# Performance work log

Measured on AMD Instinct MI355X. Metric: run time of the kernel, lower is better.

## Reference

```python
import jax, jax.numpy as jnp
import numpy as np

NA, NW, H = 20000, 100000, 128
DA, DW = 64, 128
E_CR, E_IN, E_CO = 400000, 600000, 300000


def _seg_softmax(logits, seg, n):
    m = jax.ops.segment_max(logits, seg, num_segments=n)
    e = jnp.exp(logits - m[seg])
    s = jax.ops.segment_sum(e, seg, num_segments=n)
    return e / (s[seg] + 1e-16)


def _gat(x_src, x_dst, edge, W, b, a_s, a_d):
    # PyG GATConv, heads=1, concat=False, shared lin for src/dst, add_self_loops=True
    n_src, n_dst = x_src.shape[0], x_dst.shape[0]
    loops = jnp.arange(min(n_src, n_dst), dtype=edge.dtype)
    src = jnp.concatenate([edge[0], loops])
    dst = jnp.concatenate([edge[1], loops])
    hs = x_src @ W            # [n_src, H]
    hd = x_dst @ W            # [n_dst, H]
    logit = jax.nn.leaky_relu((hs @ a_s)[src] + (hd @ a_d)[dst], 0.2)
    alpha = _seg_softmax(logit, dst, n_dst)          # softmax over in-neighborhoods
    out = jax.ops.segment_sum(alpha[:, None] * hs[src], dst, num_segments=n_dst)
    return out + b


def _mlp2(x, w1, b1, w2, b2):
    return jax.nn.relu(x @ w1 + b1) @ w2 + b2


def setup_inputs() -> dict:
    key = jax.random.key(0)
    ks = iter(jax.random.split(key, 40))

    def p(shape, scale=0.1):
        return jax.random.normal(next(ks), shape, jnp.float32) * scale

    def edges(n_src, n_dst, E):
        s = jax.random.randint(next(ks), (E,), 0, n_src, dtype=jnp.int32)
        d = jax.random.randint(next(ks), (E,), 0, n_dst, dtype=jnp.int32)
        d = jnp.where(s == d, (d + 1) % n_dst, d)  # keep input loop-free (PyG strips them)
        return jnp.stack([s, d])

    e_creates = edges(NA, NW, E_CR)
    inp = {
        'artist_feat': jax.random.normal(next(ks), (NA, DA), jnp.float32),
        'work_feat': jax.random.normal(next(ks), (NW, DW), jnp.float32),
        'a_w1': p((DA, H)), 'a_b1': jnp.zeros(H, jnp.float32),
        'a_w2': p((H, H)), 'a_b2': jnp.zeros(H, jnp.float32),
        'w_w1': p((DW, H)), 'w_b1': jnp.zeros(H, jnp.float32),
        'w_w2': p((H, H)), 'w_b2': jnp.zeros(H, jnp.float32),
        'cr_W': p((H, H)), 'cr_b': jnp.zeros(H, jnp.float32), 'cr_as': p((H,)), 'cr_ad': p((H,)),
        'in_W': p((H, H)), 'in_b': jnp.zeros(H, jnp.float32), 'in_as': p((H,)), 'in_ad': p((H,)),
        'co_W': p((H, H)), 'co_b': jnp.zeros(H, jnp.float32), 'co_as': p((H,)), 'co_ad': p((H,)),
        'p_w1': p((2 * H, 256)), 'p_b1': jnp.zeros(256, jnp.float32),
        'p_w2': p((256, 128)), 'p_b2': jnp.zeros(128, jnp.float32),
        'p_w3': p((128, 1)), 'p_b3': jnp.zeros(1, jnp.float32),
        'e_creates': e_creates,
        'e_created_by': jnp.flip(e_creates, axis=0),  # reverse relation [work, artist]
        'e_infl': edges(NW, NW, E_IN),
        'e_collab': edges(NA, NA, E_CO),
    }
    return inp


def reference(artist_feat, work_feat,
              a_w1, a_b1, a_w2, a_b2,
              w_w1, w_b1, w_w2, w_b2,
              cr_W, cr_b, cr_as, cr_ad,
              in_W, in_b, in_as, in_ad,
              co_W, co_b, co_as, co_ad,
              p_w1, p_b1, p_w2, p_b2, p_w3, p_b3,
              e_creates, e_created_by, e_infl, e_collab):
    ax = _mlp2(artist_feat, a_w1, a_b1, a_w2, a_b2)      # [NA, H]
    wx = _mlp2(work_feat, w_w1, w_b1, w_w2, w_b2)        # [NW, H]
    wx = jax.nn.elu(_gat(ax, wx, e_creates, cr_W, cr_b, cr_as, cr_ad))
    wx = jax.nn.elu(_gat(wx, wx, e_infl, in_W, in_b, in_as, in_ad))
    au = _gat(wx, ax, e_created_by, cr_W, cr_b, cr_as, cr_ad)  # no elu (matches source)
    ac = jax.nn.elu(_gat(au, au, e_collab, co_W, co_b, co_as, co_ad))
    comb = jnp.concatenate([au, ac], axis=1)             # [NA, 2H]
    h = jax.nn.relu(comb @ p_w1 + p_b1)                  # dropout is identity in eval
    h = jax.nn.relu(h @ p_w2 + p_b2)
    return (h @ p_w3 + p_b3).squeeze()
```

## Files before the change

### kernel.cpp

```cpp
#include <hip/hip_runtime.h>
#include <hip/hip_bf16.h>
#include <cstddef>

#define NA 20000
#define NW 100000
#define HH 128
#define DA 64
#define E_CR 400000
#define E_IN 600000
#define E_CO 300000

#define ROW1 0
#define ROW2 (NW)
#define ROW3 (2 * NW)
#define ROW4 (2 * NW + NA)
#define NTOT (2 * NW + 2 * NA)
#define CAPW 40
#define CAPA 88
#define NPREP (10 * 128 + 1)

typedef short v8s __attribute__((ext_vector_type(8)));
typedef float v4f __attribute__((ext_vector_type(4)));

constexpr int PSLOT = 2 * 128 * 264;

__device__ inline short f2bf(float x) {
    union { float f; unsigned u; } c; c.f = x;
    unsigned r = c.u + 0x7fff + ((c.u >> 16) & 1);
    return (short)(r >> 16);
}
__device__ inline float bf2f(short s) {
    union { unsigned u; float f; } c; c.u = ((unsigned)(unsigned short)s) << 16;
    return c.f;
}
__device__ inline float bfu2f(unsigned short s) {
    union { unsigned u; float f; } c; c.u = ((unsigned)s) << 16;
    return c.f;
}

__device__ inline void split8(const float* xv, v8s& h, v8s& l) {
#pragma unroll
    for (int p = 0; p < 4; ++p) {
        float2 xf; xf.x = xv[2 * p]; xf.y = xv[2 * p + 1];
        __hip_bfloat162 hb = __float22bfloat162_rn(xf);
        float2 hf = __bfloat1622float2(hb);
        float2 lf; lf.x = xf.x - hf.x; lf.y = xf.y - hf.y;
        __hip_bfloat162 lb = __float22bfloat162_rn(lf);
        union { __hip_bfloat162 b; short2 s; } uh, ul;
        uh.b = hb; ul.b = lb;
        h[2 * p] = uh.s.x; h[2 * p + 1] = uh.s.y;
        l[2 * p] = ul.s.x; l[2 * p + 1] = ul.s.y;
    }
}

struct AppChunk { const int* e; int E; int* pad; int cap; int* deg; };

__device__ inline void do_append(const AppChunk& ap, int bid) {
    int b0 = bid * 1024 + threadIdx.x;
    int s[4], d[4]; bool ok[4];
#pragma unroll
    for (int u = 0; u < 4; ++u) {
        int i = b0 + u * 256;
        ok[u] = i < ap.E;
        s[u] = 0; d[u] = 0;
        if (ok[u]) { s[u] = ap.e[i]; d[u] = ap.e[ap.E + i]; }
    }
    int p[4];
#pragma unroll
    for (int u = 0; u < 4; ++u) if (ok[u]) p[u] = atomicAdd(&ap.deg[d[u]], 1);
#pragma unroll
    for (int u = 0; u < 4; ++u)
        if (ok[u] && p[u] < ap.cap)
            ap.pad[(size_t)d[u] * ap.cap + p[u]] = s[u];
}

struct PrepDesc { const float* src; int ldw; int K; };
struct PrepArgs { PrepDesc d[10]; const float* wvW; const float* wvA; float* vd; };

__global__ __launch_bounds__(256) void k_prep_append(PrepArgs a, short* __restrict__ out,
                                                    AppChunk ap)
{
    if (blockIdx.x >= NPREP) { do_append(ap, blockIdx.x - NPREP); return; }
    if (blockIdx.x == NPREP - 1) {
        __shared__ float sa[HH];
        int t = threadIdx.x;
        if (t < HH) sa[t] = a.wvA[t];
        __syncthreads();
        if (t < HH) {
            float s = 0.f;
            for (int jj = 0; jj < HH; ++jj) s += a.wvW[(size_t)t * HH + jj] * sa[jj];
            a.vd[t] = s;
        }
        return;
    }
    int m = blockIdx.x >> 7;
    int e = (blockIdx.x & 127) * 256 + threadIdx.x;
    PrepDesc dd = a.d[m];
    int K = dd.K;
    int KP = (K <= 128) ? K + 8 : K;
    if (e >= K * 128) return;
    int n = e & 127, k = e >> 7;
    float x = dd.src[(size_t)k * dd.ldw + n];
    short h = f2bf(x);
    short l = f2bf(x - bf2f(h));
    short* base = out + (size_t)m * PSLOT;
    base[n * KP + k] = h;
    base[128 * KP + n * KP + k] = l;
}

template<int K, int ACT, int NSS, int ST, int LDSB, int OBF, int DUAL>
__global__ __launch_bounds__(256, 2) void k_mfma(
    const float* __restrict__ X, int ldx,
    const short* __restrict__ Wp,
    const float* __restrict__ bias,
    float* __restrict__ Y, int ldy, int M,
    const float* __restrict__ v1, float* __restrict__ ss1,
    const float* __restrict__ v2, float* __restrict__ ss2,
    const float* __restrict__ sb)
{
    constexpr int KF = K / 32;
    constexpr int KP = LDSB ? K + 8 : K;
    __shared__ short Bs[LDSB ? 2 * 128 * (K + 8) : 8];
    const int tid = threadIdx.x;
    const int wave = tid >> 6, lane = tid & 63;
    const int l15 = lane & 15, quad = lane >> 4;
    int bid = blockIdx.x;
    if (DUAL) {
        int g0 = gridDim.x >> 1;
        if (bid >= g0) { bid -= g0; Wp += PSLOT; bias += 128; Y += 128; }
    }
    const int wrow = bid * 128 + wave * 32;

    if (LDSB) {
        const float4* src = (const float4*)Wp;
        float4* dst = (float4*)Bs;
        constexpr int total = 2 * 128 * KP / 8;
        for (int i = tid; i < total; i += 256) dst[i] = src[i];
    }

    v4f acc[2][8];
#pragma unroll
    for (int rf = 0; rf < 2; ++rf)
#pragma unroll
        for (int cf = 0; cf < 8; ++cf) acc[rf][cf] = (v4f){0.f, 0.f, 0.f, 0.f};

    if (LDSB) {
        v8s ah[2][KF], al[2][KF];
#pragma unroll
        for (int rf = 0; rf < 2; ++rf) {
            int r = wrow + rf * 16 + l15; if (r >= M) r = M - 1;
            const float* xp = X + (size_t)r * ldx + quad * 8;
#pragma unroll
            for (int kf = 0; kf < KF; ++kf) {
                float xv[8];
                *(float4*)&xv[0] = *(const float4*)(xp + kf * 32);
                *(float4*)&xv[4] = *(const float4*)(xp + kf * 32 + 4);
                split8(xv, ah[rf][kf], al[rf][kf]);
            }
        }
        __syncthreads();
#pragma unroll
        for (int kf = 0; kf < KF; ++kf) {
#pragma unroll
            for (int cf = 0; cf < 8; ++cf) {
                const short* bp = &Bs[(cf * 16 + l15) * KP + kf * 32 + quad * 8];
                v8s bh = *(const v8s*)bp;
                v8s bl = *(const v8s*)(bp + 128 * KP);
#pragma unroll
                for (int rf = 0; rf < 2; ++rf) {
                    acc[rf][cf] = __builtin_amdgcn_mfma_f32_16x16x32_bf16(al[rf][kf], bh, acc[rf][cf], 0, 0, 0);
                    acc[rf][cf] = __builtin_amdgcn_mfma_f32_16x16x32_bf16(ah[rf][kf], bl, acc[rf][cf], 0, 0, 0);
                    acc[rf][cf] = __builtin_amdgcn_mfma_f32_16x16x32_bf16(ah[rf][kf], bh, acc[rf][cf], 0, 0, 0);
                }
            }
        }
    } else {
        for (int kf = 0; kf < KF; ++kf) {
            v8s ah[2], al[2];
#pragma unroll
            for (int rf = 0; rf < 2; ++rf) {
                int r = wrow + rf * 16 + l15; if (r >= M) r = M - 1;
                const float* xp = X + (size_t)r * ldx + kf * 32 + quad * 8;
                float xv[8];
                *(float4*)&xv[0] = *(const float4*)xp;
                *(float4*)&xv[4] = *(const float4*)(xp + 4);
                split8(xv, ah[rf], al[rf]);
            }
#pragma unroll
            for (int cf = 0; cf < 8; ++cf) {
                const short* bp = Wp + (size_t)(cf * 16 + l15) * K + kf * 32 + quad * 8;
                v8s bh = *(const v8s*)bp;
                v8s bl = *(const v8s*)(bp + 128 * KP);
#pragma unroll
                for (int rf = 0; rf < 2; ++rf) {
                    acc[rf][cf] = __builtin_amdgcn_mfma_f32_16x16x32_bf16(al[rf], bh, acc[rf][cf], 0, 0, 0);
                    acc[rf][cf] = __builtin_amdgcn_mfma_f32_16x16x32_bf16(ah[rf], bl, acc[rf][cf], 0, 0, 0);
                    acc[rf][cf] = __builtin_amdgcn_mfma_f32_16x16x32_bf16(ah[rf], bh, acc[rf][cf], 0, 0, 0);
                }
            }
        }
    }

    float bv[8], v1c[8], v2c[8];
#pragma unroll
    for (int cf = 0; cf < 8; ++cf) {
        int col = cf * 16 + l15;
        bv[cf] = bias ? bias[col] : 0.f;
        if (NSS >= 1) v1c[cf] = v1[col];
        if (NSS >= 2) v2c[cf] = v2[col];
    }
    float sbv = (NSS >= 1 && sb) ? sb[0] : 0.f;

#pragma unroll
    for (int rf = 0; rf < 2; ++rf) {
#pragma unroll
        for (int reg = 0; reg < 4; ++reg) {
            int r = wrow + rf * 16 + quad * 4 + reg;
            if (r >= M) continue;
            float p1 = 0.f, p2 = 0.f;
#pragma unroll
            for (int cf = 0; cf < 8; ++cf) {
                float o = acc[rf][cf][reg] + bv[cf];
                if (ACT == 1) o = o > 0.f ? o : 0.f;
                if (NSS >= 1) p1 = fmaf(o, v1c[cf], p1);
                if (NSS >= 2) p2 = fmaf(o, v2c[cf], p2);
                if (ST) {
                    if (OBF) ((unsigned short*)Y)[(size_t)r * ldy + cf * 16 + l15] = (unsigned short)f2bf(o);
                    else     Y[(size_t)r * ldy + cf * 16 + l15] = o;
                }
            }
            if (NSS >= 1) {
#pragma unroll
                for (int w = 1; w < 16; w <<= 1) {
                    p1 += __shfl_xor(p1, w, 64);
                    if (NSS >= 2) p2 += __shfl_xor(p2, w, 64);
                }
                if (l15 == 0) {
                    ss1[r] = p1 + sbv;
                    if (NSS >= 2) ss2[r] = p2;
                }
            }
        }
    }
}

struct MfmaCfg {
    const float* X; int ldx;
    const short* Wp;
    const float* bias;
    float* Y; int ldy; int M;
    int act, nss, obf;
    const float* v1; float* ss1;
    const float* v2; float* ss2;
    int nblocks;
};

__global__ __launch_bounds__(256, 2) void k_mfma2(MfmaCfg c0, MfmaCfg c1, AppChunk ap)
{
    constexpr int K = 128, KF = 4, KP = 136;
    __shared__ short Bs[2 * 128 * KP];
    int bid = blockIdx.x;
    if (bid >= c0.nblocks + c1.nblocks) { do_append(ap, bid - c0.nblocks - c1.nblocks); return; }
    const bool first = bid < c0.nblocks;
    const MfmaCfg& c = first ? c0 : c1;
    if (!first) bid -= c0.nblocks;
    const int tid = threadIdx.x;
    const int wave = tid >> 6, lane = tid & 63;
    const int l15 = lane & 15, quad = lane >> 4;
    const int wrow = bid * 128 + wave * 32;

    {
        const float4* src = (const float4*)c.Wp;
        float4* dst = (float4*)Bs;
        constexpr int total = 2 * 128 * KP / 8;
        for (int i = tid; i < total; i += 256) dst[i] = src[i];
    }

    v4f acc[2][8];
#pragma unroll
    for (int rf = 0; rf < 2; ++rf)
#pragma unroll
        for (int cf = 0; cf < 8; ++cf) acc[rf][cf] = (v4f){0.f, 0.f, 0.f, 0.f};

    v8s ah[2][KF], al[2][KF];
#pragma unroll
    for (int rf = 0; rf < 2; ++rf) {
        int r = wrow + rf * 16 + l15; if (r >= c.M) r = c.M - 1;
        const float* xp = c.X + (size_t)r * c.ldx + quad * 8;
#pragma unroll
        for (int kf = 0; kf < KF; ++kf) {
            float xv[8];
            *(float4*)&xv[0] = *(const float4*)(xp + kf * 32);
            *(float4*)&xv[4] = *(const float4*)(xp + kf * 32 + 4);
            split8(xv, ah[rf][kf], al[rf][kf]);
        }
    }
    __syncthreads();
#pragma unroll
    for (int kf = 0; kf < KF; ++kf) {
#pragma unroll
        for (int cf = 0; cf < 8; ++cf) {
            const short* bp = &Bs[(cf * 16 + l15) * KP + kf * 32 + quad * 8];
            v8s bh = *(const v8s*)bp;
            v8s bl = *(const v8s*)(bp + 128 * KP);
#pragma unroll
            for (int rf = 0; rf < 2; ++rf) {
                acc[rf][cf] = __builtin_amdgcn_mfma_f32_16x16x32_bf16(al[rf][kf], bh, acc[rf][cf], 0, 0, 0);
                acc[rf][cf] = __builtin_amdgcn_mfma_f32_16x16x32_bf16(ah[rf][kf], bl, acc[rf][cf], 0, 0, 0);
                acc[rf][cf] = __builtin_amdgcn_mfma_f32_16x16x32_bf16(ah[rf][kf], bh, acc[rf][cf], 0, 0, 0);
            }
        }
    }

    float bv[8], v1c[8], v2c[8];
#pragma unroll
    for (int cf = 0; cf < 8; ++cf) {
        int col = cf * 16 + l15;
        bv[cf] = c.bias ? c.bias[col] : 0.f;
        v1c[cf] = (c.nss >= 1) ? c.v1[col] : 0.f;
        v2c[cf] = (c.nss >= 2) ? c.v2[col] : 0.f;
    }

#pragma unroll
    for (int rf = 0; rf < 2; ++rf) {
#pragma unroll
        for (int reg = 0; reg < 4; ++reg) {
            int r = wrow + rf * 16 + quad * 4 + reg;
            if (r >= c.M) continue;
            float p1 = 0.f, p2 = 0.f;
#pragma unroll
            for (int cf = 0; cf < 8; ++cf) {
                float o = acc[rf][cf][reg] + bv[cf];
                if (c.act) o = o > 0.f ? o : 0.f;
                p1 = fmaf(o, v1c[cf], p1);
                p2 = fmaf(o, v2c[cf], p2);
                if (c.obf) ((unsigned short*)c.Y)[(size_t)r * c.ldy + cf * 16 + l15] = (unsigned short)f2bf(o);
                else       c.Y[(size_t)r * c.ldy + cf * 16 + l15] = o;
            }
            if (c.nss >= 1) {
#pragma unroll
                for (int w = 1; w < 16; w <<= 1) {
                    p1 += __shfl_xor(p1, w, 64);
                    p2 += __shfl_xor(p2, w, 64);
                }
                if (l15 == 0) {
                    c.ss1[r] = p1;
                    if (c.nss >= 2) c.ss2[r] = p2;
                }
            }
        }
    }
}

template<int ELU, int U, int CAP>
__global__ __launch_bounds__(256) void k_aggregate(
    const int* __restrict__ deg, const int* __restrict__ esp,
    const unsigned short* __restrict__ hs, const float* __restrict__ ss,
    const float* __restrict__ sd, const float* __restrict__ bias,
    float* __restrict__ out, int ldy, int n, int loopn)
{
    int lane = threadIdx.x & 63;
    int wv = threadIdx.x >> 6;
    int d = blockIdx.x * 4 + wv;
    if (d >= n) return;
    int half = lane >> 5;
    int col = (lane & 31) * 4;
    const int* row = esp + (size_t)d * CAP;
    int i1 = deg[d]; if (i1 > CAP) i1 = CAP;
    float sdv = sd[d];
    float den = 0.f;
    float ax = 0.f, ay = 0.f, az = 0.f, aw = 0.f;
    if (half == 0 && d < loopn) {
        ushort4 h = *(const ushort4*)(hs + (size_t)d * HH + col);
        float l = ss[d] + sdv;
        l = l < 0.f ? 0.2f * l : l;
        float e = __expf(l);
        den += e;
        ax = fmaf(e, bfu2f(h.x), ax);
        ay = fmaf(e, bfu2f(h.y), ay);
        az = fmaf(e, bfu2f(h.z), az);
        aw = fmaf(e, bfu2f(h.w), aw);
    }
    int i = 0;
    for (; i + 2 * U <= i1; i += 2 * U) {
        int s[U]; ushort4 h[U]; float sv[U];
#pragma unroll
        for (int u = 0; u < U; ++u) s[u] = row[i + 2 * u + half];
#pragma unroll
        for (int u = 0; u < U; ++u) h[u] = *(const ushort4*)(hs + (size_t)s[u] * HH + col);
#pragma unroll
        for (int u = 0; u < U; ++u) sv[u] = ss[s[u]];
#pragma unroll
        for (int u = 0; u < U; ++u) {
            float l = sv[u] + sdv;
            l = l < 0.f ? 0.2f * l : l;
            float e = __expf(l);
            den += e;
            ax = fmaf(e, bfu2f(h[u].x), ax);
            ay = fmaf(e, bfu2f(h[u].y), ay);
            az = fmaf(e, bfu2f(h[u].z), az);
            aw = fmaf(e, bfu2f(h[u].w), aw);
        }
    }
    if (i < i1) {
        int s[U]; ushort4 h[U]; float sv[U]; bool act[U];
#pragma unroll
        for (int u = 0; u < U; ++u) {
            int idx = i + 2 * u + half;
            act[u] = idx < i1;
            s[u] = row[act[u] ? idx : (i1 - 1)];
        }
#pragma unroll
        for (int u = 0; u < U; ++u) h[u] = *(const ushort4*)(hs + (size_t)s[u] * HH + col);
#pragma unroll
        for (int u = 0; u < U; ++u) sv[u] = ss[s[u]];
#pragma unroll
        for (int u = 0; u < U; ++u) {
            float l = sv[u] + sdv;
            l = l < 0.f ? 0.2f * l : l;
            float e = act[u] ? __expf(l) : 0.f;
            den += e;
            ax = fmaf(e, bfu2f(h[u].x), ax);
            ay = fmaf(e, bfu2f(h[u].y), ay);
            az = fmaf(e, bfu2f(h[u].z), az);
            aw = fmaf(e, bfu2f(h[u].w), aw);
        }
    }
    den += __shfl_xor(den, 32, 64);
    ax += __shfl_xor(ax, 32, 64);
    ay += __shfl_xor(ay, 32, 64);
    az += __shfl_xor(az, 32, 64);
    aw += __shfl_xor(aw, 32, 64);
    if (half == 0) {
        float4 b = *(const float4*)(bias + col);
        float inv = 1.f / (den + 1e-16f);
        float o0 = ax * inv + b.x;
        float o1 = ay * inv + b.y;
        float o2 = az * inv + b.z;
        float o3 = aw * inv + b.w;
        if (ELU) {
            o0 = o0 > 0.f ? o0 : expm1f(o0);
            o1 = o1 > 0.f ? o1 : expm1f(o1);
            o2 = o2 > 0.f ? o2 : expm1f(o2);
            o3 = o3 > 0.f ? o3 : expm1f(o3);
        }
        *(float4*)(out + (size_t)d * ldy + col) = make_float4(o0, o1, o2, o3);
    }
}

extern "C" void kernel_launch(void* const* d_in, const int* in_sizes, int n_in,
                              void* d_out, int out_size, void* d_ws, size_t ws_size,
                              hipStream_t stream)
{
    const float* artist = (const float*)d_in[0];
    const float* workf  = (const float*)d_in[1];
    const float* a_w1 = (const float*)d_in[2];  const float* a_b1 = (const float*)d_in[3];
    const float* a_w2 = (const float*)d_in[4];  const float* a_b2 = (const float*)d_in[5];
    const float* w_w1 = (const float*)d_in[6];  const float* w_b1 = (const float*)d_in[7];
    const float* w_w2 = (const float*)d_in[8];  const float* w_b2 = (const float*)d_in[9];
    const float* cr_W = (const float*)d_in[10]; const float* cr_b = (const float*)d_in[11];
    const float* cr_as = (const float*)d_in[12]; const float* cr_ad = (const float*)d_in[13];
    const float* in_W = (const float*)d_in[14]; const float* in_b = (const float*)d_in[15];
    const float* in_as = (const float*)d_in[16]; const float* in_ad = (const float*)d_in[17];
    const float* co_W = (const float*)d_in[18]; const float* co_b = (const float*)d_in[19];
    const float* co_as = (const float*)d_in[20]; const float* co_ad = (const float*)d_in[21];
    const float* p_w1 = (const float*)d_in[22]; const float* p_b1 = (const float*)d_in[23];
    const float* p_w2 = (const float*)d_in[24]; const float* p_b2 = (const float*)d_in[25];
    const float* p_w3 = (const float*)d_in[26]; const float* p_b3 = (const float*)d_in[27];
    const int* e_cr = (const int*)d_in[28];
    const int* e_cb = (const int*)d_in[29];
    const int* e_in = (const int*)d_in[30];
    const int* e_co = (const int*)d_in[31];

    char* wsp = (char*)d_ws;
    size_t off = 0;
    auto alloc = [&](size_t bytes) -> void* {
        void* p = wsp + off;
        off += (bytes + 255) / 256 * 256;
        return p;
    };
    float* ax   = (float*)alloc((size_t)NA * HH * 4);
    float* hsA  = (float*)alloc((size_t)NA * HH * 4);
    float* wx   = (float*)alloc((size_t)NW * HH * 4);
    float* hs   = (float*)alloc((size_t)NW * HH * 4);
    unsigned short* hsb = (unsigned short*)alloc((size_t)NW * HH * 2);
    float* comb = (float*)alloc((size_t)NA * 256 * 4);
    float* ss1 = (float*)alloc((size_t)NA * 4);
    float* sd1 = (float*)alloc((size_t)NW * 4);
    float* ss2 = (float*)alloc((size_t)NW * 4);
    float* sd2 = (float*)alloc((size_t)NW * 4);
    float* ss3 = (float*)alloc((size_t)NW * 4);
    float* sd3 = (float*)alloc((size_t)NA * 4);
    float* ss4 = (float*)alloc((size_t)NA * 4);
    float* sd4 = (float*)alloc((size_t)NA * 4);
    float* vd  = (float*)alloc(HH * 4);
    int* deg   = (int*)alloc((size_t)NTOT * 4);
    int* pad1  = (int*)alloc((size_t)NW * CAPW * 4);
    int* pad2  = (int*)alloc((size_t)NW * CAPW * 4);
    int* pad3  = (int*)alloc((size_t)NA * CAPA * 4);
    int* pad4  = (int*)alloc((size_t)NA * CAPA * 4);
    short* preW = (short*)alloc((size_t)10 * PSLOT * 2);
    (void)ws_size; (void)in_sizes; (void)n_in; (void)out_size;

    auto pre = [&](int m) { return preW + (size_t)m * PSLOT; };
    auto gg = [](int M) { return (M + 127) / 128; };
    auto apb = [](int E) { return (E + 1023) / 1024; };
    const float* nf = nullptr;
    float* nfm = nullptr;

    PrepArgs pa;
    pa.d[0] = {a_w1, HH, DA};
    pa.d[1] = {a_w2, HH, HH};
    pa.d[2] = {w_w1, HH, HH};
    pa.d[3] = {w_w2, HH, HH};
    pa.d[4] = {cr_W, HH, HH};
    pa.d[5] = {in_W, HH, HH};
    pa.d[6] = {co_W, HH, HH};
    pa.d[7] = {p_w1, 256, 256};
    pa.d[8] = {p_w1 + 128, 256, 256};
    pa.d[9] = {p_w2, HH, 256};
    pa.wvW = cr_W; pa.wvA = cr_ad; pa.vd = vd;

    AppChunk ap1 = {e_cr, E_CR, pad1, CAPW, deg + ROW1};
    AppChunk ap2 = {e_in, E_IN, pad2, CAPW, deg + ROW2};
    AppChunk ap3 = {e_cb, E_CR, pad3, CAPA, deg + ROW3};
    AppChunk ap4 = {e_co, E_CO, pad4, CAPA, deg + ROW4};
    AppChunk ap0 = {nullptr, 0, nullptr, 1, nullptr};

    (void)hipMemsetAsync(deg, 0, (size_t)NTOT * 4, stream);

    k_prep_append<<<NPREP + apb(E_CR), 256, 0, stream>>>(pa, preW, ap1);

    k_mfma<DA, 1, 0, 1, 1, 0, 0><<<gg(NA), 256, 0, stream>>>(artist, DA, pre(0), a_b1, hsA, HH, NA, nf, nfm, nf, nfm, nf);

    {
        MfmaCfg c0 = {workf, HH, pre(2), w_b1, hs, HH, NW, 1, 0, 0, nf, nfm, nf, nfm, gg(NW)};
        MfmaCfg c1 = {hsA, HH, pre(1), a_b2, ax, HH, NA, 0, 1, 0, vd, sd3, nf, nfm, gg(NA)};
        k_mfma2<<<gg(NW) + gg(NA) + apb(E_IN), 256, 0, stream>>>(c0, c1, ap2);
    }
    {
        MfmaCfg c0 = {hs, HH, pre(3), w_b2, wx, HH, NW, 0, 1, 0, vd, sd1, nf, nfm, gg(NW)};
        MfmaCfg c1 = {ax, HH, pre(4), nullptr, (float*)hsb, HH, NA, 0, 1, 1, cr_as, ss1, nf, nfm, gg(NA)};
        k_mfma2<<<gg(NW) + gg(NA) + apb(E_CR), 256, 0, stream>>>(c0, c1, ap3);
    }

    k_aggregate<1, 2, CAPW><<<(NW + 3) / 4, 256, 0, stream>>>(deg + ROW1, pad1, hsb, ss1, sd1, cr_b, wx, HH, NW, NA);

    {
        MfmaCfg c0 = {wx, HH, pre(5), nullptr, (float*)hsb, HH, NW, 0, 2, 1, in_as, ss2, in_ad, sd2, gg(NW)};
        MfmaCfg c1 = {nullptr, 0, nullptr, nullptr, nullptr, 0, 0, 0, 0, 0, nf, nfm, nf, nfm, 0};
        k_mfma2<<<gg(NW) + apb(E_CO), 256, 0, stream>>>(c0, c1, ap4);
    }
    k_aggregate<1, 2, CAPW><<<(NW + 3) / 4, 256, 0, stream>>>(deg + ROW2, pad2, hsb, ss2, sd2, in_b, wx, HH, NW, NW);

    k_mfma<HH, 0, 1, 1, 1, 1, 0><<<gg(NW), 256, 0, stream>>>(wx, HH, pre(4), nullptr, (float*)hsb, HH, NW, cr_as, ss3, nf, nfm, nf);
    k_aggregate<0, 4, CAPA><<<(NA + 3) / 4, 256, 0, stream>>>(deg + ROW3, pad3, hsb, ss3, sd3, cr_b, comb, 256, NA, NA);

    k_mfma<HH, 0, 2, 1, 1, 1, 0><<<gg(NA), 256, 0, stream>>>(comb, 256, pre(6), nullptr, (float*)hsb, HH, NA, co_as, ss4, co_ad, sd4, nf);
    k_aggregate<1, 4, CAPA><<<(NA + 3) / 4, 256, 0, stream>>>(deg + ROW4, pad4, hsb, ss4, sd4, co_b, comb + 128, 256, NA, NA);

    float* h1 = hs;
    k_mfma<256, 1, 0, 1, 0, 0, 1><<<2 * gg(NA), 256, 0, stream>>>(comb, 256, pre(7), p_b1, h1, 256, NA, nf, nfm, nf, nfm, nf);
    k_mfma<256, 1, 1, 0, 0, 0, 0><<<gg(NA), 256, 0, stream>>>(h1, 256, pre(9), p_b2, nfm, 0, NA, p_w3, (float*)d_out, nf, nfm, p_b3);
}
```

Measured before the change: 588.0 us.

## Halve GEMM LDS use, widen aggregate gathers to 8 bf16, rebalance edge appends

The MFMA kernels now stage only the high bf16 half of the split weights in LDS and read the low half straight from global memory, halving shared memory per block. The aggregate kernel switches from two 32-lane halves with 4-wide loads to four 16-lane quarters with 8-wide (16-byte) loads, with unroll factors reduced to match. Edge-append work is rebalanced: the influence edges are split across two fused launches via lo/hi ranges, and the artist-side projection becomes a k_mfma2 that also absorbs an append chunk. The aim is higher occupancy and better gather efficiency, at the cost of extra global/L2 traffic for the low-half weights and more cross-lane shuffles.

```diff
diff --git a/kernel.cpp b/kernel.cpp
--- a/kernel.cpp
+++ b/kernel.cpp
@@ -20,6 +20,7 @@
 #define NPREP (10 * 128 + 1)
 
 typedef short v8s __attribute__((ext_vector_type(8)));
+typedef unsigned short v8us __attribute__((ext_vector_type(8)));
 typedef float v4f __attribute__((ext_vector_type(4)));
 
 constexpr int PSLOT = 2 * 128 * 264;
@@ -53,15 +54,15 @@
     }
 }
 
-struct AppChunk { const int* e; int E; int* pad; int cap; int* deg; };
+struct AppChunk { const int* e; int E; int lo, hi; int* pad; int cap; int* deg; };
 
 __device__ inline void do_append(const AppChunk& ap, int bid) {
-    int b0 = bid * 1024 + threadIdx.x;
+    int b0 = ap.lo + bid * 1024 + threadIdx.x;
     int s[4], d[4]; bool ok[4];
 #pragma unroll
     for (int u = 0; u < 4; ++u) {
         int i = b0 + u * 256;
-        ok[u] = i < ap.E;
+        ok[u] = i < ap.hi;
         s[u] = 0; d[u] = 0;
         if (ok[u]) { s[u] = ap.e[i]; d[u] = ap.e[ap.E + i]; }
     }
@@ -120,7 +121,7 @@
 {
     constexpr int KF = K / 32;
     constexpr int KP = LDSB ? K + 8 : K;
-    __shared__ short Bs[LDSB ? 2 * 128 * (K + 8) : 8];
+    __shared__ short Bs[LDSB ? 128 * (K + 8) : 8];
     const int tid = threadIdx.x;
     const int wave = tid >> 6, lane = tid & 63;
     const int l15 = lane & 15, quad = lane >> 4;
@@ -134,7 +135,7 @@
     if (LDSB) {
         const float4* src = (const float4*)Wp;
         float4* dst = (float4*)Bs;
-        constexpr int total = 2 * 128 * KP / 8;
+        constexpr int total = 128 * KP / 8;
         for (int i = tid; i < total; i += 256) dst[i] = src[i];
     }
 
@@ -163,9 +164,9 @@
         for (int kf = 0; kf < KF; ++kf) {
 #pragma unroll
             for (int cf = 0; cf < 8; ++cf) {
-                const short* bp = &Bs[(cf * 16 + l15) * KP + kf * 32 + quad * 8];
-                v8s bh = *(const v8s*)bp;
-                v8s bl = *(const v8s*)(bp + 128 * KP);
+                int coff = (cf * 16 + l15) * KP + kf * 32 + quad * 8;
+                v8s bh = *(const v8s*)&Bs[coff];
+                v8s bl = *(const v8s*)(Wp + 128 * KP + coff);
 #pragma unroll
                 for (int rf = 0; rf < 2; ++rf) {
                     acc[rf][cf] = __builtin_amdgcn_mfma_f32_16x16x32_bf16(al[rf][kf], bh, acc[rf][cf], 0, 0, 0);
@@ -257,8 +258,8 @@
 
 __global__ __launch_bounds__(256, 2) void k_mfma2(MfmaCfg c0, MfmaCfg c1, AppChunk ap)
 {
-    constexpr int K = 128, KF = 4, KP = 136;
-    __shared__ short Bs[2 * 128 * KP];
+    constexpr int KF = 4, KP = 136;
+    __shared__ short Bs[128 * KP];
     int bid = blockIdx.x;
     if (bid >= c0.nblocks + c1.nblocks) { do_append(ap, bid - c0.nblocks - c1.nblocks); return; }
     const bool first = bid < c0.nblocks;
@@ -272,7 +273,7 @@
     {
         const float4* src = (const float4*)c.Wp;
         float4* dst = (float4*)Bs;
-        constexpr int total = 2 * 128 * KP / 8;
+        constexpr int total = 128 * KP / 8;
         for (int i = tid; i < total; i += 256) dst[i] = src[i];
     }
 
@@ -300,9 +301,9 @@
     for (int kf = 0; kf < KF; ++kf) {
 #pragma unroll
         for (int cf = 0; cf < 8; ++cf) {
-            const short* bp = &Bs[(cf * 16 + l15) * KP + kf * 32 + quad * 8];
-            v8s bh = *(const v8s*)bp;
-            v8s bl = *(const v8s*)(bp + 128 * KP);
+            int coff = (cf * 16 + l15) * KP + kf * 32 + quad * 8;
+            v8s bh = *(const v8s*)&Bs[coff];
+            v8s bl = *(const v8s*)(c.Wp + 128 * KP + coff);
 #pragma unroll
             for (int rf = 0; rf < 2; ++rf) {
                 acc[rf][cf] = __builtin_amdgcn_mfma_f32_16x16x32_bf16(al[rf][kf], bh, acc[rf][cf], 0, 0, 0);
@@ -363,31 +364,31 @@
     int wv = threadIdx.x >> 6;
     int d = blockIdx.x * 4 + wv;
     if (d >= n) return;
-    int half = lane >> 5;
-    int col = (lane & 31) * 4;
+    int q = lane >> 4;
+    int col = (lane & 15) * 8;
     const int* row = esp + (size_t)d * CAP;
     int i1 = deg[d]; if (i1 > CAP) i1 = CAP;
     float sdv = sd[d];
     float den = 0.f;
-    float ax = 0.f, ay = 0.f, az = 0.f, aw = 0.f;
-    if (half == 0 && d < loopn) {
-        ushort4 h = *(const ushort4*)(hs + (size_t)d * HH + col);
+    float acc[8];
+#pragma unroll
+    for (int j = 0; j < 8; ++j) acc[j] = 0.f;
+    if (q == 0 && d < loopn) {
+        v8us h = *(const v8us*)(hs + (size_t)d * HH + col);
         float l = ss[d] + sdv;
         l = l < 0.f ? 0.2f * l : l;
         float e = __expf(l);
         den += e;
-        ax = fmaf(e, bfu2f(h.x), ax);
-        ay = fmaf(e, bfu2f(h.y), ay);
-        az = fmaf(e, bfu2f(h.z), az);
-        aw = fmaf(e, bfu2f(h.w), aw);
+#pragma unroll
+        for (int j = 0; j < 8; ++j) acc[j] = fmaf(e, bfu2f(h[j]), acc[j]);
     }
     int i = 0;
-    for (; i + 2 * U <= i1; i += 2 * U) {
-        int s[U]; ushort4 h[U]; float sv[U];
-#pragma unroll
-        for (int u = 0; u < U; ++u) s[u] = row[i + 2 * u + half];
-#pragma unroll
-        for (int u = 0; u < U; ++u) h[u] = *(const ushort4*)(hs + (size_t)s[u] * HH + col);
+    for (; i + 4 * U <= i1; i += 4 * U) {
+        int s[U]; v8us h[U]; float sv[U];
+#pragma unroll
+        for (int u = 0; u < U; ++u) s[u] = row[i + 4 * u + q];
+#pragma unroll
+        for (int u = 0; u < U; ++u) h[u] = *(const v8us*)(hs + (size_t)s[u] * HH + col);
 #pragma unroll
         for (int u = 0; u < U; ++u) sv[u] = ss[s[u]];
 #pragma unroll
@@ -396,22 +397,20 @@
             l = l < 0.f ? 0.2f * l : l;
             float e = __expf(l);
             den += e;
-            ax = fmaf(e, bfu2f(h[u].x), ax);
-            ay = fmaf(e, bfu2f(h[u].y), ay);
-            az = fmaf(e, bfu2f(h[u].z), az);
-            aw = fmaf(e, bfu2f(h[u].w), aw);
+#pragma unroll
+            for (int j = 0; j < 8; ++j) acc[j] = fmaf(e, bfu2f(h[u][j]), acc[j]);
         }
     }
     if (i < i1) {
-        int s[U]; ushort4 h[U]; float sv[U]; bool act[U];
+        int s[U]; v8us h[U]; float sv[U]; bool act[U];
 #pragma unroll
         for (int u = 0; u < U; ++u) {
-            int idx = i + 2 * u + half;
+            int idx = i + 4 * u + q;
             act[u] = idx < i1;
             s[u] = row[act[u] ? idx : (i1 - 1)];
         }
 #pragma unroll
-        for (int u = 0; u < U; ++u) h[u] = *(const ushort4*)(hs + (size_t)s[u] * HH + col);
+        for (int u = 0; u < U; ++u) h[u] = *(const v8us*)(hs + (size_t)s[u] * HH + col);
 #pragma unroll
         for (int u = 0; u < U; ++u) sv[u] = ss[s[u]];
 #pragma unroll
@@ -420,31 +419,27 @@
             l = l < 0.f ? 0.2f * l : l;
             float e = act[u] ? __expf(l) : 0.f;
             den += e;
-            ax = fmaf(e, bfu2f(h[u].x), ax);
-            ay = fmaf(e, bfu2f(h[u].y), ay);
-            az = fmaf(e, bfu2f(h[u].z), az);
-            aw = fmaf(e, bfu2f(h[u].w), aw);
-        }
-    }
+#pragma unroll
+            for (int j = 0; j < 8; ++j) acc[j] = fmaf(e, bfu2f(h[u][j]), acc[j]);
+        }
+    }
+    den += __shfl_xor(den, 16, 64);
     den += __shfl_xor(den, 32, 64);
-    ax += __shfl_xor(ax, 32, 64);
-    ay += __shfl_xor(ay, 32, 64);
-    az += __shfl_xor(az, 32, 64);
-    aw += __shfl_xor(aw, 32, 64);
-    if (half == 0) {
-        float4 b = *(const float4*)(bias + col);
+#pragma unroll
+    for (int j = 0; j < 8; ++j) {
+        acc[j] += __shfl_xor(acc[j], 16, 64);
+        acc[j] += __shfl_xor(acc[j], 32, 64);
+    }
+    if (q == 0) {
         float inv = 1.f / (den + 1e-16f);
-        float o0 = ax * inv + b.x;
-        float o1 = ay * inv + b.y;
-        float o2 = az * inv + b.z;
-        float o3 = aw * inv + b.w;
-        if (ELU) {
-            o0 = o0 > 0.f ? o0 : expm1f(o0);
-            o1 = o1 > 0.f ? o1 : expm1f(o1);
-            o2 = o2 > 0.f ? o2 : expm1f(o2);
-            o3 = o3 > 0.f ? o3 : expm1f(o3);
-        }
-        *(float4*)(out + (size_t)d * ldy + col) = make_float4(o0, o1, o2, o3);
+        float o[8];
+#pragma unroll
+        for (int j = 0; j < 8; ++j) {
+            o[j] = acc[j] * inv + bias[col + j];
+            if (ELU) o[j] = o[j] > 0.f ? o[j] : expm1f(o[j]);
+        }
+        *(float4*)(out + (size_t)d * ldy + col) = *(float4*)&o[0];
+        *(float4*)(out + (size_t)d * ldy + col + 4) = *(float4*)&o[4];
     }
 }
 
@@ -504,7 +499,7 @@
 
     auto pre = [&](int m) { return preW + (size_t)m * PSLOT; };
     auto gg = [](int M) { return (M + 127) / 128; };
-    auto apb = [](int E) { return (E + 1023) / 1024; };
+    auto apb = [](int lo, int hi) { return (hi - lo + 1023) / 1024; };
     const float* nf = nullptr;
     float* nfm = nullptr;
 
@@ -521,43 +516,48 @@
     pa.d[9] = {p_w2, HH, 256};
     pa.wvW = cr_W; pa.wvA = cr_ad; pa.vd = vd;
 
-    AppChunk ap1 = {e_cr, E_CR, pad1, CAPW, deg + ROW1};
-    AppChunk ap2 = {e_in, E_IN, pad2, CAPW, deg + ROW2};
-    AppChunk ap3 = {e_cb, E_CR, pad3, CAPA, deg + ROW3};
-    AppChunk ap4 = {e_co, E_CO, pad4, CAPA, deg + ROW4};
-    AppChunk ap0 = {nullptr, 0, nullptr, 1, nullptr};
+    const int EHALF = 300000;
+    AppChunk ap1  = {e_cr, E_CR, 0, E_CR, pad1, CAPW, deg + ROW1};
+    AppChunk ap2a = {e_in, E_IN, 0, EHALF, pad2, CAPW, deg + ROW2};
+    AppChunk ap2b = {e_in, E_IN, EHALF, E_IN, pad2, CAPW, deg + ROW2};
+    AppChunk ap3  = {e_cb, E_CR, 0, E_CR, pad3, CAPA, deg + ROW3};
+    AppChunk ap4  = {e_co, E_CO, 0, E_CO, pad4, CAPA, deg + ROW4};
 
     (void)hipMemsetAsync(deg, 0, (size_t)NTOT * 4, stream);
 
-    k_prep_append<<<NPREP + apb(E_CR), 256, 0, stream>>>(pa, preW, ap1);
+    k_prep_append<<<NPREP + apb(0, E_CR), 256, 0, stream>>>(pa, preW, ap1);
 
     k_mfma<DA, 1, 0, 1, 1, 0, 0><<<gg(NA), 256, 0, stream>>>(artist, DA, pre(0), a_b1, hsA, HH, NA, nf, nfm, nf, nfm, nf);
 
     {
         MfmaCfg c0 = {workf, HH, pre(2), w_b1, hs, HH, NW, 1, 0, 0, nf, nfm, nf, nfm, gg(NW)};
         MfmaCfg c1 = {hsA, HH, pre(1), a_b2, ax, HH, NA, 0, 1, 0, vd, sd3, nf, nfm, gg(NA)};
-        k_mfma2<<<gg(NW) + gg(NA) + apb(E_IN), 256, 0, stream>>>(c0, c1, ap2);
+        k_mfma2<<<gg(NW) + gg(NA) + apb(0, EHALF), 256, 0, stream>>>(c0, c1, ap2a);
     }
     {
         MfmaCfg c0 = {hs, HH, pre(3), w_b2, wx, HH, NW, 0, 1, 0, vd, sd1, nf, nfm, gg(NW)};
         MfmaCfg c1 = {ax, HH, pre(4), nullptr, (float*)hsb, HH, NA, 0, 1, 1, cr_as, ss1, nf, nfm, gg(NA)};
-        k_mfma2<<<gg(NW) + gg(NA) + apb(E_CR), 256, 0, stream>>>(c0, c1, ap3);
-    }
-
-    k_aggregate<1, 2, CAPW><<<(NW + 3) / 4, 256, 0, stream>>>(deg + ROW1, pad1, hsb, ss1, sd1, cr_b, wx, HH, NW, NA);
+        k_mfma2<<<gg(NW) + gg(NA) + apb(EHALF, E_IN), 256, 0, stream>>>(c0, c1, ap2b);
+    }
+
+    k_aggregate<1, 1, CAPW><<<(NW + 3) / 4, 256, 0, stream>>>(deg + ROW1, pad1, hsb, ss1, sd1, cr_b, wx, HH, NW, NA);
 
     {
         MfmaCfg c0 = {wx, HH, pre(5), nullptr, (float*)hsb, HH, NW, 0, 2, 1, in_as, ss2, in_ad, sd2, gg(NW)};
         MfmaCfg c1 = {nullptr, 0, nullptr, nullptr, nullptr, 0, 0, 0, 0, 0, nf, nfm, nf, nfm, 0};
-        k_mfma2<<<gg(NW) + apb(E_CO), 256, 0, stream>>>(c0, c1, ap4);
-    }
-    k_aggregate<1, 2, CAPW><<<(NW + 3) / 4, 256, 0, stream>>>(deg + ROW2, pad2, hsb, ss2, sd2, in_b, wx, HH, NW, NW);
-
-    k_mfma<HH, 0, 1, 1, 1, 1, 0><<<gg(NW), 256, 0, stream>>>(wx, HH, pre(4), nullptr, (float*)hsb, HH, NW, cr_as, ss3, nf, nfm, nf);
-    k_aggregate<0, 4, CAPA><<<(NA + 3) / 4, 256, 0, stream>>>(deg + ROW3, pad3, hsb, ss3, sd3, cr_b, comb, 256, NA, NA);
+        k_mfma2<<<gg(NW) + apb(0, E_CR), 256, 0, stream>>>(c0, c1, ap3);
+    }
+    k_aggregate<1, 1, CAPW><<<(NW + 3) / 4, 256, 0, stream>>>(deg + ROW2, pad2, hsb, ss2, sd2, in_b, wx, HH, NW, NW);
+
+    {
+        MfmaCfg c0 = {wx, HH, pre(4), nullptr, (float*)hsb, HH, NW, 0, 1, 1, cr_as, ss3, nf, nfm, gg(NW)};
+        MfmaCfg c1 = {nullptr, 0, nullptr, nullptr, nullptr, 0, 0, 0, 0, 0, nf, nfm, nf, nfm, 0};
+        k_mfma2<<<gg(NW) + apb(0, E_CO), 256, 0, stream>>>(c0, c1, ap4);
+    }
+    k_aggregate<0, 2, CAPA><<<(NA + 3) / 4, 256, 0, stream>>>(deg + ROW3, pad3, hsb, ss3, sd3, cr_b, comb, 256, NA, NA);
 
     k_mfma<HH, 0, 2, 1, 1, 1, 0><<<gg(NA), 256, 0, stream>>>(comb, 256, pre(6), nullptr, (float*)hsb, HH, NA, co_as, ss4, co_ad, sd4, nf);
-    k_aggregate<1, 4, CAPA><<<(NA + 3) / 4, 256, 0, stream>>>(deg + ROW4, pad4, hsb, ss4, sd4, co_b, comb + 128, 256, NA, NA);
+    k_aggregate<1, 2, CAPA><<<(NA + 3) / 4, 256, 0, stream>>>(deg + ROW4, pad4, hsb, ss4, sd4, co_b, comb + 128, 256, NA, NA);
 
     float* h1 = hs;
     k_mfma<256, 1, 0, 1, 0, 0, 1><<<2 * gg(NA), 256, 0, stream>>>(comb, 256, pre(7), p_b1, h1, 256, NA, nf, nfm, nf, nfm, nf);
```

Measured after the change: 688.3 us. +17.1%, slower.

## Rebalance edge-append work across fused GEMM launches and halve LDS weight staging

Applied to the files above, without the earlier changes.

The edge-bucketing (append) work is redistributed. The influence edges are split into two halves that piggyback on the first two fused GEMM launches, and the created_by and collab appends move to later GEMM launches (the latter now a fused k_mfma2 launch). Separately, only the high bf16 half of the split weights is staged in LDS, while the low half is read straight from global memory. This halves shared memory per block, which may allow more blocks per CU, at the cost of extra global or L2 loads in the MFMA inner loop.

```diff
diff --git a/kernel.cpp b/kernel.cpp
--- a/kernel.cpp
+++ b/kernel.cpp
@@ -53,15 +53,15 @@
     }
 }
 
-struct AppChunk { const int* e; int E; int* pad; int cap; int* deg; };
+struct AppChunk { const int* e; int E; int lo, hi; int* pad; int cap; int* deg; };
 
 __device__ inline void do_append(const AppChunk& ap, int bid) {
-    int b0 = bid * 1024 + threadIdx.x;
+    int b0 = ap.lo + bid * 1024 + threadIdx.x;
     int s[4], d[4]; bool ok[4];
 #pragma unroll
     for (int u = 0; u < 4; ++u) {
         int i = b0 + u * 256;
-        ok[u] = i < ap.E;
+        ok[u] = i < ap.hi;
         s[u] = 0; d[u] = 0;
         if (ok[u]) { s[u] = ap.e[i]; d[u] = ap.e[ap.E + i]; }
     }
@@ -120,7 +120,7 @@
 {
     constexpr int KF = K / 32;
     constexpr int KP = LDSB ? K + 8 : K;
-    __shared__ short Bs[LDSB ? 2 * 128 * (K + 8) : 8];
+    __shared__ short Bs[LDSB ? 128 * (K + 8) : 8];
     const int tid = threadIdx.x;
     const int wave = tid >> 6, lane = tid & 63;
     const int l15 = lane & 15, quad = lane >> 4;
@@ -134,7 +134,7 @@
     if (LDSB) {
         const float4* src = (const float4*)Wp;
         float4* dst = (float4*)Bs;
-        constexpr int total = 2 * 128 * KP / 8;
+        constexpr int total = 128 * KP / 8;
         for (int i = tid; i < total; i += 256) dst[i] = src[i];
     }
 
@@ -163,9 +163,9 @@
         for (int kf = 0; kf < KF; ++kf) {
 #pragma unroll
             for (int cf = 0; cf < 8; ++cf) {
-                const short* bp = &Bs[(cf * 16 + l15) * KP + kf * 32 + quad * 8];
-                v8s bh = *(const v8s*)bp;
-                v8s bl = *(const v8s*)(bp + 128 * KP);
+                int coff = (cf * 16 + l15) * KP + kf * 32 + quad * 8;
+                v8s bh = *(const v8s*)&Bs[coff];
+                v8s bl = *(const v8s*)(Wp + 128 * KP + coff);
 #pragma unroll
                 for (int rf = 0; rf < 2; ++rf) {
                     acc[rf][cf] = __builtin_amdgcn_mfma_f32_16x16x32_bf16(al[rf][kf], bh, acc[rf][cf], 0, 0, 0);
@@ -257,8 +257,8 @@
 
 __global__ __launch_bounds__(256, 2) void k_mfma2(MfmaCfg c0, MfmaCfg c1, AppChunk ap)
 {
-    constexpr int K = 128, KF = 4, KP = 136;
-    __shared__ short Bs[2 * 128 * KP];
+    constexpr int KF = 4, KP = 136;
+    __shared__ short Bs[128 * KP];
     int bid = blockIdx.x;
     if (bid >= c0.nblocks + c1.nblocks) { do_append(ap, bid - c0.nblocks - c1.nblocks); return; }
     const bool first = bid < c0.nblocks;
@@ -272,7 +272,7 @@
     {
         const float4* src = (const float4*)c.Wp;
         float4* dst = (float4*)Bs;
-        constexpr int total = 2 * 128 * KP / 8;
+        constexpr int total = 128 * KP / 8;
         for (int i = tid; i < total; i += 256) dst[i] = src[i];
     }
 
@@ -300,9 +300,9 @@
     for (int kf = 0; kf < KF; ++kf) {
 #pragma unroll
         for (int cf = 0; cf < 8; ++cf) {
-            const short* bp = &Bs[(cf * 16 + l15) * KP + kf * 32 + quad * 8];
-            v8s bh = *(const v8s*)bp;
-            v8s bl = *(const v8s*)(bp + 128 * KP);
+            int coff = (cf * 16 + l15) * KP + kf * 32 + quad * 8;
+            v8s bh = *(const v8s*)&Bs[coff];
+            v8s bl = *(const v8s*)(c.Wp + 128 * KP + coff);
 #pragma unroll
             for (int rf = 0; rf < 2; ++rf) {
                 acc[rf][cf] = __builtin_amdgcn_mfma_f32_16x16x32_bf16(al[rf][kf], bh, acc[rf][cf], 0, 0, 0);
@@ -504,7 +504,7 @@
 
     auto pre = [&](int m) { return preW + (size_t)m * PSLOT; };
     auto gg = [](int M) { return (M + 127) / 128; };
-    auto apb = [](int E) { return (E + 1023) / 1024; };
+    auto apb = [](int lo, int hi) { return (hi - lo + 1023) / 1024; };
     const float* nf = nullptr;
     float* nfm = nullptr;
 
@@ -521,27 +521,28 @@
     pa.d[9] = {p_w2, HH, 256};
     pa.wvW = cr_W; pa.wvA = cr_ad; pa.vd = vd;
 
-    AppChunk ap1 = {e_cr, E_CR, pad1, CAPW, deg + ROW1};
-    AppChunk ap2 = {e_in, E_IN, pad2, CAPW, deg + ROW2};
-    AppChunk ap3 = {e_cb, E_CR, pad3, CAPA, deg + ROW3};
-    AppChunk ap4 = {e_co, E_CO, pad4, CAPA, deg + ROW4};
-    AppChunk ap0 = {nullptr, 0, nullptr, 1, nullptr};
+    const int EHALF = 300000;
+    AppChunk ap1  = {e_cr, E_CR, 0, E_CR, pad1, CAPW, deg + ROW1};
+    AppChunk ap2a = {e_in, E_IN, 0, EHALF, pad2, CAPW, deg + ROW2};
+    AppChunk ap2b = {e_in, E_IN, EHALF, E_IN, pad2, CAPW, deg + ROW2};
+    AppChunk ap3  = {e_cb, E_CR, 0, E_CR, pad3, CAPA, deg + ROW3};
+    AppChunk ap4  = {e_co, E_CO, 0, E_CO, pad4, CAPA, deg + ROW4};
 
     (void)hipMemsetAsync(deg, 0, (size_t)NTOT * 4, stream);
 
-    k_prep_append<<<NPREP + apb(E_CR), 256, 0, stream>>>(pa, preW, ap1);
+    k_prep_append<<<NPREP + apb(0, E_CR), 256, 0, stream>>>(pa, preW, ap1);
 
     k_mfma<DA, 1, 0, 1, 1, 0, 0><<<gg(NA), 256, 0, stream>>>(artist, DA, pre(0), a_b1, hsA, HH, NA, nf, nfm, nf, nfm, nf);
 
     {
         MfmaCfg c0 = {workf, HH, pre(2), w_b1, hs, HH, NW, 1, 0, 0, nf, nfm, nf, nfm, gg(NW)};
         MfmaCfg c1 = {hsA, HH, pre(1), a_b2, ax, HH, NA, 0, 1, 0, vd, sd3, nf, nfm, gg(NA)};
-        k_mfma2<<<gg(NW) + gg(NA) + apb(E_IN), 256, 0, stream>>>(c0, c1, ap2);
+        k_mfma2<<<gg(NW) + gg(NA) + apb(0, EHALF), 256, 0, stream>>>(c0, c1, ap2a);
     }
     {
         MfmaCfg c0 = {hs, HH, pre(3), w_b2, wx, HH, NW, 0, 1, 0, vd, sd1, nf, nfm, gg(NW)};
         MfmaCfg c1 = {ax, HH, pre(4), nullptr, (float*)hsb, HH, NA, 0, 1, 1, cr_as, ss1, nf, nfm, gg(NA)};
-        k_mfma2<<<gg(NW) + gg(NA) + apb(E_CR), 256, 0, stream>>>(c0, c1, ap3);
+        k_mfma2<<<gg(NW) + gg(NA) + apb(EHALF, E_IN), 256, 0, stream>>>(c0, c1, ap2b);
     }
 
     k_aggregate<1, 2, CAPW><<<(NW + 3) / 4, 256, 0, stream>>>(deg + ROW1, pad1, hsb, ss1, sd1, cr_b, wx, HH, NW, NA);
@@ -549,11 +550,15 @@
     {
         MfmaCfg c0 = {wx, HH, pre(5), nullptr, (float*)hsb, HH, NW, 0, 2, 1, in_as, ss2, in_ad, sd2, gg(NW)};
         MfmaCfg c1 = {nullptr, 0, nullptr, nullptr, nullptr, 0, 0, 0, 0, 0, nf, nfm, nf, nfm, 0};
-        k_mfma2<<<gg(NW) + apb(E_CO), 256, 0, stream>>>(c0, c1, ap4);
+        k_mfma2<<<gg(NW) + apb(0, E_CR), 256, 0, stream>>>(c0, c1, ap3);
     }
     k_aggregate<1, 2, CAPW><<<(NW + 3) / 4, 256, 0, stream>>>(deg + ROW2, pad2, hsb, ss2, sd2, in_b, wx, HH, NW, NW);
 
-    k_mfma<HH, 0, 1, 1, 1, 1, 0><<<gg(NW), 256, 0, stream>>>(wx, HH, pre(4), nullptr, (float*)hsb, HH, NW, cr_as, ss3, nf, nfm, nf);
+    {
+        MfmaCfg c0 = {wx, HH, pre(4), nullptr, (float*)hsb, HH, NW, 0, 1, 1, cr_as, ss3, nf, nfm, gg(NW)};
+        MfmaCfg c1 = {nullptr, 0, nullptr, nullptr, nullptr, 0, 0, 0, 0, 0, nf, nfm, nf, nfm, 0};
+        k_mfma2<<<gg(NW) + apb(0, E_CO), 256, 0, stream>>>(c0, c1, ap4);
+    }
     k_aggregate<0, 4, CAPA><<<(NA + 3) / 4, 256, 0, stream>>>(deg + ROW3, pad3, hsb, ss3, sd3, cr_b, comb, 256, NA, NA);
 
     k_mfma<HH, 0, 2, 1, 1, 1, 0><<<gg(NA), 256, 0, stream>>>(comb, 256, pre(6), nullptr, (float*)hsb, HH, NA, co_as, ss4, co_ad, sd4, nf);
```

New measurement: 631.6 us. 7.4% more time.
